# Performance work log

Hardware: AMD Instinct MI355X
Metric: run time of the kernel (lower is better)

The kernel has to match this reference:

```python
import jax, jax.numpy as jnp
import numpy as np

N_NODES = 50000
N_EDGES = 640000
D_IN = 128
D_OUT = 128


def setup_inputs() -> dict:
    key = jax.random.key(0)
    k1, k2, k3, k4 = jax.random.split(key, 4)
    x = jax.random.normal(k1, (N_NODES, D_IN), dtype=jnp.float32)
    edge_index = jax.random.randint(k2, (2, N_EDGES), 0, N_NODES, dtype=jnp.int64)
    weight = jax.random.uniform(k3, (1,), dtype=jnp.float32)
    temperature = jnp.ones((1,), dtype=jnp.float32)
    W = jax.random.normal(k4, (D_IN, D_OUT), dtype=jnp.float32) * (1.0 / np.sqrt(D_IN))
    b = jnp.zeros((D_OUT,), dtype=jnp.float32)
    return {"x": x, "edge_index": edge_index, "weight": weight,
            "temperature": temperature, "W": W, "b": b}


def _gcn_conv(x, edge_index, W, b):
    N = x.shape[0]
    src, dst = edge_index[0], edge_index[1]
    loop = jnp.arange(N, dtype=edge_index.dtype)
    s = jnp.concatenate([src, loop])  # self-loops appended
    d = jnp.concatenate([dst, loop])
    deg = jax.ops.segment_sum(jnp.ones(s.shape[0], dtype=x.dtype), d, num_segments=N)
    dinv = jnp.where(deg > 0, deg ** -0.5, 0.0)
    norm = dinv[s] * dinv[d]  # [E+N]
    h = x @ W                 # linear transform first (PyG GCNConv)
    msg = h[s] * norm[:, None]
    out = jax.ops.segment_sum(msg, d, num_segments=N)
    return out + b


def _gradient_entropy(x, edge_index, temperature):
    # Boltzmann distribution over per-node Dirichlet energies;
    # entropy gradient w.r.t. node features (computed with autodiff).
    N = x.shape[0]
    src, dst = edge_index[0], edge_index[1]

    def entropy(z):
        diff = z[src] - z[dst]                                  # [E, D]
        E = jax.ops.segment_sum(jnp.sum(diff * diff, axis=-1), dst, num_segments=N)
        logp = jax.nn.log_softmax(-E / temperature[0])
        p = jnp.exp(logp)
        return -jnp.sum(p * logp)

    return jax.grad(entropy)(x)


def reference(x, edge_index, weight, temperature, W, b):
    h = _gcn_conv(x, edge_index, W, b)
    g = jax.lax.stop_gradient(_gradient_entropy(h, edge_index, temperature))
    return h + weight * g
```

## Files before the change

kernel.cpp:

```cpp
#include <hip/hip_runtime.h>

#define N_NODES 50000
#define N_EDGES 640000
#define NSCANB  196
#define MAXD    64
#define NBUCK   196
#define BUCKCAP 4096
#define EPB     2048
#define NPARTB  313

#define OFF_HTMPB    0
#define OFF_OBF      3200000
#define OFF_DEG      6400000
#define OFF_DINV     6450000
#define OFF_E        6500000
#define OFF_PMIN     6550000
#define OFF_PS0      6550256
#define OFF_PS1      6550512
#define OFF_WT       6550768
#define OFF_GCUR     6558960
#define OFF_PART     6559216
#define OFF_EBIN     7362032

typedef __attribute__((ext_vector_type(8))) short bf16x8;
typedef __attribute__((ext_vector_type(4))) float f32x4;

__device__ __forceinline__ unsigned short f2bf(float f) {
    unsigned u = __float_as_uint(f);
    unsigned r = u + 0x7fffu + ((u >> 16) & 1u);
    return (unsigned short)(r >> 16);
}
__device__ __forceinline__ float bflo(unsigned u) { return __uint_as_float(u << 16); }
__device__ __forceinline__ float bfhi(unsigned u) { return __uint_as_float(u & 0xffff0000u); }

__global__ __launch_bounds__(256) void k_init(const float* __restrict__ W,
                                              int* __restrict__ gcursor,
                                              unsigned short* __restrict__ wtg) {
    int gtid = blockIdx.x * 256 + threadIdx.x;
    if (gtid < NBUCK) gcursor[gtid] = 0;
    if (gtid < 4096) {
        int k = gtid >> 5, n4 = (gtid & 31) * 4;
        float4 v = *(const float4*)(W + k * 128 + n4);
        wtg[(n4 + 0) * 128 + k] = f2bf(v.x);
        wtg[(n4 + 1) * 128 + k] = f2bf(v.y);
        wtg[(n4 + 2) * 128 + k] = f2bf(v.z);
        wtg[(n4 + 3) * 128 + k] = f2bf(v.w);
    }
}

__global__ __launch_bounds__(256) void k_part(const int* __restrict__ src,
                                              const int* __restrict__ dst,
                                              int* __restrict__ gcursor,
                                              unsigned* __restrict__ part) {
    __shared__ int hist[NBUCK];
    __shared__ int base[NBUCK];
    int tid = threadIdx.x;
    if (tid < NBUCK) hist[tid] = 0;
    __syncthreads();
    int e0 = blockIdx.x * EPB;
    unsigned val[8]; int bk[8]; int rk[8];
    #pragma unroll
    for (int j = 0; j < 8; j++) {
        int e = e0 + j * 256 + tid;
        if (e < N_EDGES) {
            int s = src[e], d = dst[e];
            int bc = d >> 8;
            if ((unsigned)bc >= NBUCK) bc = NBUCK - 1;
            bk[j] = bc;
            val[j] = ((unsigned)(d & 255) << 16) | ((unsigned)s & 0xffffu);
            rk[j] = atomicAdd(&hist[bc], 1);
        } else { bk[j] = -1; val[j] = 0u; rk[j] = 0; }
    }
    __syncthreads();
    if (tid < NBUCK) base[tid] = atomicAdd(&gcursor[tid], hist[tid]);
    __syncthreads();
    #pragma unroll
    for (int j = 0; j < 8; j++) {
        if (bk[j] >= 0) {
            int p = base[bk[j]] + rk[j];
            if ((unsigned)p < BUCKCAP) part[bk[j] * BUCKCAP + p] = val[j];
        }
    }
}

__global__ __launch_bounds__(256) void k_bin(const int* __restrict__ gcursor,
                                             const unsigned* __restrict__ part,
                                             unsigned short* __restrict__ ebin,
                                             int* __restrict__ deg,
                                             float* __restrict__ dinv) {
    __shared__ __align__(16) unsigned short bins[256][MAXD];
    __shared__ int cnt[256];
    int tid = threadIdx.x, bkt = blockIdx.x;
    cnt[tid] = 0;
    __syncthreads();
    int M = gcursor[bkt];
    if (M > BUCKCAP) M = BUCKCAP;
    if (M < 0) M = 0;
    for (int i = tid; i < M; i += 256) {
        unsigned v = part[bkt * BUCKCAP + i];
        int ln = (v >> 16) & 255;
        int pos = atomicAdd(&cnt[ln], 1);
        if (pos < MAXD) bins[ln][pos] = (unsigned short)(v & 0xffffu);
    }
    __syncthreads();
    int node = bkt * 256 + tid;
    if (node < N_NODES) {
        int dg = cnt[tid]; if (dg > MAXD) dg = MAXD;
        deg[node] = dg;
        dinv[node] = rsqrtf((float)(dg + 1));
    }
    int nvalid = N_NODES - bkt * 256; if (nvalid > 256) nvalid = 256;
    if (nvalid < 0) nvalid = 0;
    int lim = nvalid * MAXD / 8;
    const uint4* bs = (const uint4*)&bins[0][0];
    uint4* gb = (uint4*)(ebin + (size_t)bkt * 256 * MAXD);
    for (int i = tid; i < lim; i += 256) gb[i] = bs[i];
}

__global__ __launch_bounds__(256) void k_gemm(const float* __restrict__ x,
                                              const unsigned short* __restrict__ wtg,
                                              const float* __restrict__ dinv,
                                              unsigned short* __restrict__ htmpb) {
    int tid = threadIdx.x;
    int wave = tid >> 6, lane = tid & 63, quad = lane >> 4, m16 = lane & 15;
    int r0 = blockIdx.x * 32 + (wave & 1) * 16;
    int ch = (wave >> 1) * 4;
    int arow = r0 + m16;
    int rowc = arow < N_NODES ? arow : N_NODES - 1;
    f32x4 acc[4];
    #pragma unroll
    for (int c = 0; c < 4; c++) acc[c] = (f32x4){0.f, 0.f, 0.f, 0.f};
    #pragma unroll
    for (int kt = 0; kt < 4; kt++) {
        int koff = kt * 32 + quad * 8;
        float4 xa = *(const float4*)(x + rowc * 128 + koff);
        float4 xb = *(const float4*)(x + rowc * 128 + koff + 4);
        bf16x8 af;
        af[0] = (short)f2bf(xa.x); af[1] = (short)f2bf(xa.y);
        af[2] = (short)f2bf(xa.z); af[3] = (short)f2bf(xa.w);
        af[4] = (short)f2bf(xb.x); af[5] = (short)f2bf(xb.y);
        af[6] = (short)f2bf(xb.z); af[7] = (short)f2bf(xb.w);
        #pragma unroll
        for (int c = 0; c < 4; c++) {
            bf16x8 bfrag = *(const bf16x8*)(wtg + ((ch + c) * 16 + m16) * 128 + koff);
            acc[c] = __builtin_amdgcn_mfma_f32_16x16x32_bf16(af, bfrag, acc[c], 0, 0, 0);
        }
    }
    #pragma unroll
    for (int reg = 0; reg < 4; reg++) {
        int grow = r0 + quad * 4 + reg;
        if (grow < N_NODES) {
            float dv = dinv[grow];
            #pragma unroll
            for (int c = 0; c < 4; c++)
                htmpb[grow * 128 + (ch + c) * 16 + m16] = f2bf(acc[c][reg] * dv);
        }
    }
}

__global__ __launch_bounds__(256) void k_gather(const unsigned short* __restrict__ htmpb,
                                                const int* __restrict__ deg,
                                                const float* __restrict__ dinv,
                                                const float* __restrict__ b,
                                                const unsigned short* __restrict__ ebin,
                                                float* __restrict__ out,
                                                unsigned short* __restrict__ obf) {
    int node = blockIdx.x * 8 + (threadIdx.x >> 5);
    int lane = threadIdx.x & 31;
    int dg = deg[node]; if (dg > MAXD) dg = MAXD; if (dg < 0) dg = 0;
    float di = dinv[node];
    float4 bv = *(const float4*)(b + lane * 4);
    uint2 hv = *(const uint2*)(htmpb + node * 128 + lane * 4);
    float ax = bflo(hv.x), ay = bfhi(hv.x), az = bflo(hv.y), aw = bfhi(hv.y);
    float cx = 0.f, cy = 0.f, cz = 0.f, cw = 0.f;
    const unsigned short* bin = ebin + node * MAXD;
    int k = 0;
    for (; k + 3 < dg; k += 4) {
        uint2 bw = *(const uint2*)(bin + k);
        int s0 = bw.x & 0xffff, s1 = bw.x >> 16;
        int s2 = bw.y & 0xffff, s3 = bw.y >> 16;
        uint2 u0 = *(const uint2*)(htmpb + s0 * 128 + lane * 4);
        uint2 u1 = *(const uint2*)(htmpb + s1 * 128 + lane * 4);
        uint2 u2 = *(const uint2*)(htmpb + s2 * 128 + lane * 4);
        uint2 u3 = *(const uint2*)(htmpb + s3 * 128 + lane * 4);
        ax += bflo(u0.x); ay += bfhi(u0.x); az += bflo(u0.y); aw += bfhi(u0.y);
        cx += bflo(u1.x); cy += bfhi(u1.x); cz += bflo(u1.y); cw += bfhi(u1.y);
        ax += bflo(u2.x); ay += bfhi(u2.x); az += bflo(u2.y); aw += bfhi(u2.y);
        cx += bflo(u3.x); cy += bfhi(u3.x); cz += bflo(u3.y); cw += bfhi(u3.y);
    }
    for (; k < dg; k++) {
        int s0 = bin[k];
        uint2 u0 = *(const uint2*)(htmpb + s0 * 128 + lane * 4);
        ax += bflo(u0.x); ay += bfhi(u0.x); az += bflo(u0.y); aw += bfhi(u0.y);
    }
    ax += cx; ay += cy; az += cz; aw += cw;
    ax = bv.x + di * ax; ay = bv.y + di * ay;
    az = bv.z + di * az; aw = bv.w + di * aw;
    *(float4*)(out + node * 128 + lane * 4) = make_float4(ax, ay, az, aw);
    uint2 pk;
    pk.x = (unsigned)f2bf(ax) | ((unsigned)f2bf(ay) << 16);
    pk.y = (unsigned)f2bf(az) | ((unsigned)f2bf(aw) << 16);
    *(uint2*)(obf + node * 128 + lane * 4) = pk;
}

__global__ __launch_bounds__(256) void k_energy(const unsigned short* __restrict__ obf,
                                                const int* __restrict__ deg,
                                                const unsigned short* __restrict__ ebin,
                                                float* __restrict__ E) {
    int node = blockIdx.x * 8 + (threadIdx.x >> 5);
    int lane = threadIdx.x & 31;
    int dg = deg[node]; if (dg > MAXD) dg = MAXD; if (dg < 0) dg = 0;
    uint2 ud = *(const uint2*)(obf + node * 128 + lane * 4);
    float o0 = bflo(ud.x), o1 = bfhi(ud.x), o2 = bflo(ud.y), o3 = bfhi(ud.y);
    float acc = 0.f, acc2 = 0.f;
    const unsigned short* bin = ebin + node * MAXD;
    int k = 0;
    for (; k + 3 < dg; k += 4) {
        uint2 bw = *(const uint2*)(bin + k);
        int s0 = bw.x & 0xffff, s1 = bw.x >> 16;
        int s2 = bw.y & 0xffff, s3 = bw.y >> 16;
        uint2 a = *(const uint2*)(obf + s0 * 128 + lane * 4);
        uint2 c = *(const uint2*)(obf + s1 * 128 + lane * 4);
        uint2 g = *(const uint2*)(obf + s2 * 128 + lane * 4);
        uint2 h = *(const uint2*)(obf + s3 * 128 + lane * 4);
        float d0 = bflo(a.x) - o0, d1 = bfhi(a.x) - o1, d2 = bflo(a.y) - o2, d3 = bfhi(a.y) - o3;
        float e4 = bflo(c.x) - o0, e5 = bfhi(c.x) - o1, e6 = bflo(c.y) - o2, e7 = bfhi(c.y) - o3;
        float f0 = bflo(g.x) - o0, f1 = bfhi(g.x) - o1, f2 = bflo(g.y) - o2, f3 = bfhi(g.y) - o3;
        float h4 = bflo(h.x) - o0, h5 = bfhi(h.x) - o1, h6 = bflo(h.y) - o2, h7 = bfhi(h.y) - o3;
        acc  += d0 * d0 + d1 * d1 + d2 * d2 + d3 * d3;
        acc2 += e4 * e4 + e5 * e5 + e6 * e6 + e7 * e7;
        acc  += f0 * f0 + f1 * f1 + f2 * f2 + f3 * f3;
        acc2 += h4 * h4 + h5 * h5 + h6 * h6 + h7 * h7;
    }
    for (; k < dg; k++) {
        int s0 = bin[k];
        uint2 a = *(const uint2*)(obf + s0 * 128 + lane * 4);
        float d0 = bflo(a.x) - o0, d1 = bfhi(a.x) - o1, d2 = bflo(a.y) - o2, d3 = bfhi(a.y) - o3;
        acc += d0 * d0 + d1 * d1 + d2 * d2 + d3 * d3;
    }
    acc += acc2;
    #pragma unroll
    for (int off = 16; off; off >>= 1) acc += __shfl_xor(acc, off);
    if (lane == 0) E[node] = acc;
}

__global__ __launch_bounds__(256) void k_esoft(const float* __restrict__ E,
                                               const float* __restrict__ temp,
                                               float* __restrict__ pmin,
                                               float* __restrict__ ps0,
                                               float* __restrict__ ps1) {
    __shared__ float fred[12];
    int tid = threadIdx.x;
    int i = blockIdx.x * 256 + tid;
    int lane = tid & 63, wid = tid >> 6;
    float e = (i < N_NODES) ? E[i] : 3.402823466e38f;
    float m = e;
    #pragma unroll
    for (int off = 32; off; off >>= 1) m = fminf(m, __shfl_xor(m, off));
    if (lane == 0) fred[wid] = m;
    __syncthreads();
    float bm = fminf(fminf(fred[0], fred[1]), fminf(fred[2], fred[3]));
    float T = temp[0];
    float s0 = 0.f, s1 = 0.f;
    if (i < N_NODES) {
        float dd = (bm - e) / T;
        float ed = __expf(dd);
        s0 = ed; s1 = ed * dd;
    }
    #pragma unroll
    for (int off = 32; off; off >>= 1) { s0 += __shfl_xor(s0, off); s1 += __shfl_xor(s1, off); }
    __syncthreads();
    if (lane == 0) { fred[4 + wid] = s0; fred[8 + wid] = s1; }
    __syncthreads();
    if (tid == 0) {
        pmin[blockIdx.x] = bm;
        ps0[blockIdx.x] = fred[4] + fred[5] + fred[6] + fred[7];
        ps1[blockIdx.x] = fred[8] + fred[9] + fred[10] + fred[11];
    }
}

__global__ __launch_bounds__(256) void k_grad(const int* __restrict__ deg,
                                              const unsigned short* __restrict__ ebin,
                                              const float* __restrict__ E,
                                              const float* __restrict__ temp,
                                              const float* __restrict__ pmin,
                                              const float* __restrict__ ps0,
                                              const float* __restrict__ ps1,
                                              const float* __restrict__ weight,
                                              float* __restrict__ out) {
    __shared__ float fred[12];
    int tid = threadIdx.x;
    int lane = tid & 63, wid = tid >> 6;

    float pm = (tid < NSCANB) ? pmin[tid] : 3.402823466e38f;
    float m = pm;
    #pragma unroll
    for (int off = 32; off; off >>= 1) m = fminf(m, __shfl_xor(m, off));
    if (lane == 0) fred[wid] = m;
    __syncthreads();
    float gmin = fminf(fminf(fred[0], fred[1]), fminf(fred[2], fred[3]));
    float T = temp[0];
    float s0 = 0.f, s1 = 0.f;
    if (tid < NSCANB) {
        float dl = (gmin - pm) / T;
        float ex = __expf(dl);
        float b0 = ps0[tid], b1 = ps1[tid];
        s0 = ex * b0;
        s1 = ex * (b1 + dl * b0);
    }
    #pragma unroll
    for (int off = 32; off; off >>= 1) { s0 += __shfl_xor(s0, off); s1 += __shfl_xor(s1, off); }
    __syncthreads();
    if (lane == 0) { fred[4 + wid] = s0; fred[8 + wid] = s1; }
    __syncthreads();
    float S0 = fred[4] + fred[5] + fred[6] + fred[7];
    float S1 = fred[8] + fred[9] + fred[10] + fred[11];

    float wscale = 2.f * weight[0];
    int lane32 = tid & 31;
    int node = blockIdx.x * 8 + (tid >> 5);
    if (node >= N_NODES) return;
    float dd = (gmin - E[node]) / T;
    float qd = (__expf(dd) / S0) * (dd - S1 / S0) / T;
    if (qd == 0.f) return;
    float cc = wscale * qd;
    int dg = deg[node]; if (dg > MAXD) dg = MAXD; if (dg < 0) dg = 0;
    float4 od = *(const float4*)(out + node * 128 + lane32 * 4);
    float sx = 0.f, sy = 0.f, sz = 0.f, sw = 0.f;
    const unsigned short* bin = ebin + node * MAXD;
    for (int k = 0; k < dg; k++) {
        int s = bin[k];
        if (s >= N_NODES) s = N_NODES - 1;
        float4 a = *(const float4*)(out + s * 128 + lane32 * 4);
        float vx = cc * (a.x - od.x), vy = cc * (a.y - od.y);
        float vz = cc * (a.z - od.z), vw = cc * (a.w - od.w);
        float* os = out + s * 128 + lane32 * 4;
        atomicAdd(os + 0, vx); atomicAdd(os + 1, vy);
        atomicAdd(os + 2, vz); atomicAdd(os + 3, vw);
        sx += vx; sy += vy; sz += vz; sw += vw;
    }
    float* odp = out + node * 128 + lane32 * 4;
    atomicAdd(odp + 0, -sx); atomicAdd(odp + 1, -sy);
    atomicAdd(odp + 2, -sz); atomicAdd(odp + 3, -sw);
}

extern "C" void kernel_launch(void* const* d_in, const int* in_sizes, int n_in,
                              void* d_out, int out_size, void* d_ws, size_t ws_size,
                              hipStream_t stream) {
    const float* x      = (const float*)d_in[0];
    const int*   ei     = (const int*)d_in[1];
    const float* weight = (const float*)d_in[2];
    const float* temp   = (const float*)d_in[3];
    const float* W      = (const float*)d_in[4];
    const float* b      = (const float*)d_in[5];
    float* out = (float*)d_out;
    float* ws  = (float*)d_ws;

    const int* src = ei;
    const int* dst = ei + N_EDGES;

    unsigned short* htmpb = (unsigned short*)(ws + OFF_HTMPB);
    unsigned short* obf   = (unsigned short*)(ws + OFF_OBF);
    int*   deg      = (int*)(ws + OFF_DEG);
    float* dinv     = ws + OFF_DINV;
    float* Earr     = ws + OFF_E;
    float* pminA    = ws + OFF_PMIN;
    float* ps0A     = ws + OFF_PS0;
    float* ps1A     = ws + OFF_PS1;
    unsigned short* wtg = (unsigned short*)(ws + OFF_WT);
    int*   gcursor  = (int*)(ws + OFF_GCUR);
    unsigned* part  = (unsigned*)(ws + OFF_PART);
    unsigned short* ebin = (unsigned short*)(ws + OFF_EBIN);

    k_init<<<16, 256, 0, stream>>>(W, gcursor, wtg);
    k_part<<<NPARTB, 256, 0, stream>>>(src, dst, gcursor, part);
    k_bin<<<NBUCK, 256, 0, stream>>>(gcursor, part, ebin, deg, dinv);
    k_gemm<<<1563, 256, 0, stream>>>(x, wtg, dinv, htmpb);
    k_gather<<<6250, 256, 0, stream>>>(htmpb, deg, dinv, b, ebin, out, obf);
    k_energy<<<6250, 256, 0, stream>>>(obf, deg, ebin, Earr);
    k_esoft<<<NSCANB, 256, 0, stream>>>(Earr, temp, pminA, ps0A, ps1A);
    k_grad<<<6250, 256, 0, stream>>>(deg, ebin, Earr, temp, pminA, ps0A, ps1A, weight, out);
}
```

Measured before the change: 218.0 us.

## Split bf16 feature matrices into column slices to shrink gather working set

Stores the bf16 hidden and output features as four 32-column slices, each contiguous over nodes, and launches the gather and energy kernels once per slice with 16 lanes per node. Each slice's working set is a quarter of the full matrix, so the random neighbour gathers are meant to hit in L2/MALL more often. Partial energies per slice are written separately and summed in the softmax-statistics kernel. In exchange the launches have four times as many blocks, each neighbour load is narrower (4 bytes per lane), and the edge lists and degrees are re-read once per slice.

```diff
diff --git a/kernel.cpp b/kernel.cpp
--- a/kernel.cpp
+++ b/kernel.cpp
@@ -8,19 +8,23 @@
 #define BUCKCAP 4096
 #define EPB     2048
 #define NPARTB  313
+#define NSLICE  4
+#define NGB     3125
+#define SLICE_STRIDE 1600000
 
 #define OFF_HTMPB    0
 #define OFF_OBF      3200000
 #define OFF_DEG      6400000
 #define OFF_DINV     6450000
-#define OFF_E        6500000
-#define OFF_PMIN     6550000
-#define OFF_PS0      6550256
-#define OFF_PS1      6550512
-#define OFF_WT       6550768
-#define OFF_GCUR     6558960
-#define OFF_PART     6559216
-#define OFF_EBIN     7362032
+#define OFF_E4       6500000
+#define OFF_EF       6700000
+#define OFF_PMIN     6750000
+#define OFF_PS0      6750256
+#define OFF_PS1      6750512
+#define OFF_WT       6750768
+#define OFF_GCUR     6758960
+#define OFF_PART     6759216
+#define OFF_EBIN     7562032
 
 typedef __attribute__((ext_vector_type(8))) short bf16x8;
 typedef __attribute__((ext_vector_type(4))) float f32x4;
@@ -152,8 +156,11 @@
         if (grow < N_NODES) {
             float dv = dinv[grow];
             #pragma unroll
-            for (int c = 0; c < 4; c++)
-                htmpb[grow * 128 + (ch + c) * 16 + m16] = f2bf(acc[c][reg] * dv);
+            for (int c = 0; c < 4; c++) {
+                int col = (ch + c) * 16 + m16;
+                htmpb[(col >> 5) * SLICE_STRIDE + grow * 32 + (col & 31)]
+                    = f2bf(acc[c][reg] * dv);
+            }
         }
     }
 }
@@ -165,53 +172,58 @@
                                                 const unsigned short* __restrict__ ebin,
                                                 float* __restrict__ out,
                                                 unsigned short* __restrict__ obf) {
-    int node = blockIdx.x * 8 + (threadIdx.x >> 5);
-    int lane = threadIdx.x & 31;
+    int bs = blockIdx.x;
+    int slice = bs / NGB, nb = bs - slice * NGB;
+    int node = nb * 16 + (threadIdx.x >> 4);
+    int lane16 = threadIdx.x & 15;
+    const unsigned short* hs = htmpb + slice * SLICE_STRIDE;
     int dg = deg[node]; if (dg > MAXD) dg = MAXD; if (dg < 0) dg = 0;
     float di = dinv[node];
-    float4 bv = *(const float4*)(b + lane * 4);
-    uint2 hv = *(const uint2*)(htmpb + node * 128 + lane * 4);
-    float ax = bflo(hv.x), ay = bfhi(hv.x), az = bflo(hv.y), aw = bfhi(hv.y);
-    float cx = 0.f, cy = 0.f, cz = 0.f, cw = 0.f;
+    float2 bv = *(const float2*)(b + slice * 32 + lane16 * 2);
+    unsigned hv = *(const unsigned*)(hs + node * 32 + lane16 * 2);
+    float ax = bflo(hv), ay = bfhi(hv);
+    float cx = 0.f, cy = 0.f;
     const unsigned short* bin = ebin + node * MAXD;
+    int c2 = lane16 * 2;
     int k = 0;
     for (; k + 3 < dg; k += 4) {
         uint2 bw = *(const uint2*)(bin + k);
         int s0 = bw.x & 0xffff, s1 = bw.x >> 16;
         int s2 = bw.y & 0xffff, s3 = bw.y >> 16;
-        uint2 u0 = *(const uint2*)(htmpb + s0 * 128 + lane * 4);
-        uint2 u1 = *(const uint2*)(htmpb + s1 * 128 + lane * 4);
-        uint2 u2 = *(const uint2*)(htmpb + s2 * 128 + lane * 4);
-        uint2 u3 = *(const uint2*)(htmpb + s3 * 128 + lane * 4);
-        ax += bflo(u0.x); ay += bfhi(u0.x); az += bflo(u0.y); aw += bfhi(u0.y);
-        cx += bflo(u1.x); cy += bfhi(u1.x); cz += bflo(u1.y); cw += bfhi(u1.y);
-        ax += bflo(u2.x); ay += bfhi(u2.x); az += bflo(u2.y); aw += bfhi(u2.y);
-        cx += bflo(u3.x); cy += bfhi(u3.x); cz += bflo(u3.y); cw += bfhi(u3.y);
+        unsigned u0 = *(const unsigned*)(hs + s0 * 32 + c2);
+        unsigned u1 = *(const unsigned*)(hs + s1 * 32 + c2);
+        unsigned u2 = *(const unsigned*)(hs + s2 * 32 + c2);
+        unsigned u3 = *(const unsigned*)(hs + s3 * 32 + c2);
+        ax += bflo(u0); ay += bfhi(u0);
+        cx += bflo(u1); cy += bfhi(u1);
+        ax += bflo(u2); ay += bfhi(u2);
+        cx += bflo(u3); cy += bfhi(u3);
     }
     for (; k < dg; k++) {
         int s0 = bin[k];
-        uint2 u0 = *(const uint2*)(htmpb + s0 * 128 + lane * 4);
-        ax += bflo(u0.x); ay += bfhi(u0.x); az += bflo(u0.y); aw += bfhi(u0.y);
-    }
-    ax += cx; ay += cy; az += cz; aw += cw;
+        unsigned u0 = *(const unsigned*)(hs + s0 * 32 + c2);
+        ax += bflo(u0); ay += bfhi(u0);
+    }
+    ax += cx; ay += cy;
     ax = bv.x + di * ax; ay = bv.y + di * ay;
-    az = bv.z + di * az; aw = bv.w + di * aw;
-    *(float4*)(out + node * 128 + lane * 4) = make_float4(ax, ay, az, aw);
-    uint2 pk;
-    pk.x = (unsigned)f2bf(ax) | ((unsigned)f2bf(ay) << 16);
-    pk.y = (unsigned)f2bf(az) | ((unsigned)f2bf(aw) << 16);
-    *(uint2*)(obf + node * 128 + lane * 4) = pk;
+    *(float2*)(out + node * 128 + slice * 32 + c2) = make_float2(ax, ay);
+    unsigned pk = (unsigned)f2bf(ax) | ((unsigned)f2bf(ay) << 16);
+    *(unsigned*)(obf + slice * SLICE_STRIDE + node * 32 + c2) = pk;
 }
 
 __global__ __launch_bounds__(256) void k_energy(const unsigned short* __restrict__ obf,
                                                 const int* __restrict__ deg,
                                                 const unsigned short* __restrict__ ebin,
-                                                float* __restrict__ E) {
-    int node = blockIdx.x * 8 + (threadIdx.x >> 5);
-    int lane = threadIdx.x & 31;
+                                                float* __restrict__ E4) {
+    int bs = blockIdx.x;
+    int slice = bs / NGB, nb = bs - slice * NGB;
+    int node = nb * 16 + (threadIdx.x >> 4);
+    int lane16 = threadIdx.x & 15;
+    const unsigned short* os = obf + slice * SLICE_STRIDE;
     int dg = deg[node]; if (dg > MAXD) dg = MAXD; if (dg < 0) dg = 0;
-    uint2 ud = *(const uint2*)(obf + node * 128 + lane * 4);
-    float o0 = bflo(ud.x), o1 = bfhi(ud.x), o2 = bflo(ud.y), o3 = bfhi(ud.y);
+    int c2 = lane16 * 2;
+    unsigned ud = *(const unsigned*)(os + node * 32 + c2);
+    float o0 = bflo(ud), o1 = bfhi(ud);
     float acc = 0.f, acc2 = 0.f;
     const unsigned short* bin = ebin + node * MAXD;
     int k = 0;
@@ -219,33 +231,34 @@
         uint2 bw = *(const uint2*)(bin + k);
         int s0 = bw.x & 0xffff, s1 = bw.x >> 16;
         int s2 = bw.y & 0xffff, s3 = bw.y >> 16;
-        uint2 a = *(const uint2*)(obf + s0 * 128 + lane * 4);
-        uint2 c = *(const uint2*)(obf + s1 * 128 + lane * 4);
-        uint2 g = *(const uint2*)(obf + s2 * 128 + lane * 4);
-        uint2 h = *(const uint2*)(obf + s3 * 128 + lane * 4);
-        float d0 = bflo(a.x) - o0, d1 = bfhi(a.x) - o1, d2 = bflo(a.y) - o2, d3 = bfhi(a.y) - o3;
-        float e4 = bflo(c.x) - o0, e5 = bfhi(c.x) - o1, e6 = bflo(c.y) - o2, e7 = bfhi(c.y) - o3;
-        float f0 = bflo(g.x) - o0, f1 = bfhi(g.x) - o1, f2 = bflo(g.y) - o2, f3 = bfhi(g.y) - o3;
-        float h4 = bflo(h.x) - o0, h5 = bfhi(h.x) - o1, h6 = bflo(h.y) - o2, h7 = bfhi(h.y) - o3;
-        acc  += d0 * d0 + d1 * d1 + d2 * d2 + d3 * d3;
-        acc2 += e4 * e4 + e5 * e5 + e6 * e6 + e7 * e7;
-        acc  += f0 * f0 + f1 * f1 + f2 * f2 + f3 * f3;
-        acc2 += h4 * h4 + h5 * h5 + h6 * h6 + h7 * h7;
+        unsigned a = *(const unsigned*)(os + s0 * 32 + c2);
+        unsigned c = *(const unsigned*)(os + s1 * 32 + c2);
+        unsigned g = *(const unsigned*)(os + s2 * 32 + c2);
+        unsigned h = *(const unsigned*)(os + s3 * 32 + c2);
+        float d0 = bflo(a) - o0, d1 = bfhi(a) - o1;
+        float e0 = bflo(c) - o0, e1 = bfhi(c) - o1;
+        float f0 = bflo(g) - o0, f1 = bfhi(g) - o1;
+        float g0 = bflo(h) - o0, g1 = bfhi(h) - o1;
+        acc  += d0 * d0 + d1 * d1;
+        acc2 += e0 * e0 + e1 * e1;
+        acc  += f0 * f0 + f1 * f1;
+        acc2 += g0 * g0 + g1 * g1;
     }
     for (; k < dg; k++) {
         int s0 = bin[k];
-        uint2 a = *(const uint2*)(obf + s0 * 128 + lane * 4);
-        float d0 = bflo(a.x) - o0, d1 = bfhi(a.x) - o1, d2 = bflo(a.y) - o2, d3 = bfhi(a.y) - o3;
-        acc += d0 * d0 + d1 * d1 + d2 * d2 + d3 * d3;
+        unsigned a = *(const unsigned*)(os + s0 * 32 + c2);
+        float d0 = bflo(a) - o0, d1 = bfhi(a) - o1;
+        acc += d0 * d0 + d1 * d1;
     }
     acc += acc2;
     #pragma unroll
-    for (int off = 16; off; off >>= 1) acc += __shfl_xor(acc, off);
-    if (lane == 0) E[node] = acc;
-}
-
-__global__ __launch_bounds__(256) void k_esoft(const float* __restrict__ E,
+    for (int off = 8; off; off >>= 1) acc += __shfl_xor(acc, off);
+    if (lane16 == 0) E4[slice * N_NODES + node] = acc;
+}
+
+__global__ __launch_bounds__(256) void k_esoft(const float* __restrict__ E4,
                                                const float* __restrict__ temp,
+                                               float* __restrict__ Efin,
                                                float* __restrict__ pmin,
                                                float* __restrict__ ps0,
                                                float* __restrict__ ps1) {
@@ -253,7 +266,11 @@
     int tid = threadIdx.x;
     int i = blockIdx.x * 256 + tid;
     int lane = tid & 63, wid = tid >> 6;
-    float e = (i < N_NODES) ? E[i] : 3.402823466e38f;
+    float e = 3.402823466e38f;
+    if (i < N_NODES) {
+        e = E4[i] + E4[N_NODES + i] + E4[2 * N_NODES + i] + E4[3 * N_NODES + i];
+        Efin[i] = e;
+    }
     float m = e;
     #pragma unroll
     for (int off = 32; off; off >>= 1) m = fminf(m, __shfl_xor(m, off));
@@ -363,7 +380,8 @@
     unsigned short* obf   = (unsigned short*)(ws + OFF_OBF);
     int*   deg      = (int*)(ws + OFF_DEG);
     float* dinv     = ws + OFF_DINV;
-    float* Earr     = ws + OFF_E;
+    float* E4       = ws + OFF_E4;
+    float* Efin     = ws + OFF_EF;
     float* pminA    = ws + OFF_PMIN;
     float* ps0A     = ws + OFF_PS0;
     float* ps1A     = ws + OFF_PS1;
@@ -376,8 +394,8 @@
     k_part<<<NPARTB, 256, 0, stream>>>(src, dst, gcursor, part);
     k_bin<<<NBUCK, 256, 0, stream>>>(gcursor, part, ebin, deg, dinv);
     k_gemm<<<1563, 256, 0, stream>>>(x, wtg, dinv, htmpb);
-    k_gather<<<6250, 256, 0, stream>>>(htmpb, deg, dinv, b, ebin, out, obf);
-    k_energy<<<6250, 256, 0, stream>>>(obf, deg, ebin, Earr);
-    k_esoft<<<NSCANB, 256, 0, stream>>>(Earr, temp, pminA, ps0A, ps1A);
-    k_grad<<<6250, 256, 0, stream>>>(deg, ebin, Earr, temp, pminA, ps0A, ps1A, weight, out);
-}
+    k_gather<<<NSLICE * NGB, 256, 0, stream>>>(htmpb, deg, dinv, b, ebin, out, obf);
+    k_energy<<<NSLICE * NGB, 256, 0, stream>>>(obf, deg, ebin, E4);
+    k_esoft<<<NSCANB, 256, 0, stream>>>(E4, temp, Efin, pminA, ps0A, ps1A);
+    k_grad<<<6250, 256, 0, stream>>>(deg, ebin, Efin, temp, pminA, ps0A, ps1A, weight, out);
+}
```

Measured after the change: 239.7 us. 1.1x slower.
